# Kernel tuning notes

Measured on AMD Instinct MI355X. Metric: run time of the kernel, lower is better.

The kernel has to match this reference:

```python
import jax, jax.numpy as jnp
import numpy as np

N = 16384      # nodes
E = 524288     # edges (avg degree 32)
F_IN = 128     # input features
H1 = 256       # first_gcn_dimensions
H2 = 256       # second_gcn_dimensions
D1 = 64        # first_dense_neurons
D2 = 2         # second_dense_neurons (fixed by EYE=ones(2))


def setup_inputs() -> dict:
    key = jax.random.key(0)
    ks = jax.random.split(key, 8)
    w = lambda k, shp: (jax.random.normal(k, shp, jnp.float32) * 0.05)
    return dict(
        features=jax.random.normal(ks[0], (N, F_IN), jnp.float32),
        edges=jax.random.randint(ks[1], (2, E), 0, N),
        W1=w(ks[2], (F_IN, H1)), b1=jnp.zeros((H1,), jnp.float32),
        W2=w(ks[3], (H1, H2)), b2=jnp.zeros((H2,), jnp.float32),
        fc1_w=w(ks[4], (D1, H2)), fc1_b=jnp.zeros((D1,), jnp.float32),
        fc2_w=w(ks[5], (D2, D1)), fc2_b=jnp.zeros((D2,), jnp.float32),
    )


def gcn_conv(x, W, b, src, dst, n):
    """PyG GCNConv: xW, add self-loops, symmetric D^-1/2 (A+I) D^-1/2 aggregation."""
    x = x @ W
    loops = jnp.arange(n)
    s = jnp.concatenate([src, loops])
    d = jnp.concatenate([dst, loops])
    deg = jax.ops.segment_sum(jnp.ones(s.shape, x.dtype), d, num_segments=n)
    dinv = jnp.where(deg > 0, jax.lax.rsqrt(deg), 0.0)
    msg = x[s] * (dinv[s] * dinv[d])[:, None]          # gather + scale
    return jax.ops.segment_sum(msg, d, num_segments=n) + b  # scatter-add


def reference(features, edges, W1, b1, W2, b2, fc1_w, fc1_b, fc2_w, fc2_b):
    n = features.shape[0]
    src, dst = edges[0], edges[1]
    h1 = jax.nn.relu(gcn_conv(features, W1, b1, src, dst, n))
    h2 = gcn_conv(h1, W2, b2, src, dst, n)                 # [N, H2]
    a1 = jnp.tanh(h2 @ fc1_w.T + fc1_b)                    # [N, D1]
    assignment = jax.nn.softmax(a1 @ fc2_w.T + fc2_b, axis=1)  # [N, 2]
    group_features = assignment.T @ h2                     # [2, H2]
    # to_dense_adj: dense NxN adjacency, duplicate edges accumulate
    adj = jnp.zeros((n, n), h2.dtype).at[src, dst].add(1.0)
    new_adj = assignment.T @ (adj @ assignment)            # [2, 2]
    positive = jnp.clip(group_features[0][None, :], -100.0, 100.0)
    negative = jnp.clip(group_features[1][None, :], -100.0, 100.0)
    # F.normalize(p=1, dim=1) with eps=1e-12
    denom = jnp.maximum(jnp.sum(jnp.abs(new_adj), axis=1, keepdims=True), 1e-12)
    norm_diag = jnp.diag(new_adj / denom)
    pos_penalty = jnp.mean((norm_diag - 1.0) ** 2)         # MSE vs ones(2)
    graph_embedding = jnp.mean(group_features, axis=0, keepdims=True)  # [1, H2]
    return (graph_embedding, positive, negative, pos_penalty)
```

## Files before the change

### kernel.cpp

```cpp
#include <hip/hip_runtime.h>
#include <hip/hip_bf16.h>
#include <math.h>

#define N_NODES 16384
#define N_EDGES 524288
#define F_IN 128
#define H1 256
#define H2 256
#define D1 64
#define NA_GRID 128
#define DEG_CAP 96

typedef __attribute__((ext_vector_type(8))) short short8;
typedef __attribute__((ext_vector_type(4))) float floatx4;
typedef unsigned short ushort_t;
typedef unsigned int uint_t;

__device__ inline float bf2f(ushort_t u) {
    union { uint_t i; float f; } v;
    v.i = ((uint_t)u) << 16;
    return v.f;
}
__device__ inline float u2f_lo(uint_t u) {
    union { uint_t i; float f; } v;
    v.i = u << 16;
    return v.f;
}
__device__ inline float u2f_hi(uint_t u) {
    union { uint_t i; float f; } v;
    v.i = u & 0xffff0000u;
    return v.f;
}
__device__ inline ushort_t f2bs(float x) {
    __hip_bfloat16 h = __float2bfloat16(x);
    return *reinterpret_cast<ushort_t*>(&h);
}

__global__ __launch_bounds__(256) void prep_fill(
    const int* __restrict__ src, const int* __restrict__ dst,
    const float* __restrict__ W1, const float* __restrict__ W2,
    const float* __restrict__ fc1_w,
    int* __restrict__ cur, int* __restrict__ col,
    ushort_t* __restrict__ W1t, ushort_t* __restrict__ W2t,
    ushort_t* __restrict__ fc1bf) {
    int b = blockIdx.x, t = threadIdx.x;
    if (b < 2048) {
        int e = b * 256 + t;
        int d = dst[e];
        int pos = atomicAdd(&cur[d], 1);
        if (pos < DEG_CAP) col[d * DEG_CAP + pos] = src[e];
    } else if (b < 2176) {
        int idx = (b - 2048) * 256 + t;
        int n = idx >> 7, k = idx & 127;
        W1t[idx] = f2bs(W1[k * 256 + n]);
    } else if (b < 2432) {
        int idx = (b - 2176) * 256 + t;
        int n = idx >> 8, k = idx & 255;
        W2t[idx] = f2bs(W2[k * 256 + n]);
    } else {
        int idx = (b - 2432) * 256 + t;
        fc1bf[idx] = f2bs(fc1_w[idx]);
    }
}

__global__ __launch_bounds__(256) void scale_feat(
    const float* __restrict__ features, const int* __restrict__ cnt,
    ushort_t* __restrict__ zs) {
    int gid = blockIdx.x * 256 + threadIdx.x;
    int node = gid >> 5;
    float d = rsqrtf((float)(cnt[node] + 1));
    float4 v = *(const float4*)&features[gid * 4];
    uint2 p;
    p.x = (uint_t)f2bs(v.x * d) | ((uint_t)f2bs(v.y * d) << 16);
    p.y = (uint_t)f2bs(v.z * d) | ((uint_t)f2bs(v.w * d) << 16);
    *(uint2*)&zs[gid * 4] = p;
}

__global__ __launch_bounds__(512, 8) void fused_layer1(
    const ushort_t* __restrict__ zs, const int* __restrict__ cnt,
    const int* __restrict__ col, const float* __restrict__ b1,
    const ushort_t* __restrict__ W1t, const ushort_t* __restrict__ W2t,
    ushort_t* __restrict__ bufY) {
    __shared__ __align__(16) ushort_t Az[16 * 136];
    __shared__ __align__(16) ushort_t Ah[16 * 264];
    const int tid = threadIdx.x;
    const int lane = tid & 63;
    const int wave = tid >> 6;
    const int m = lane & 15;
    const int quad = lane >> 4;
    const int row0 = blockIdx.x * 16;

    for (int ii = 0; ii < 2; ++ii) {
        const int nl = wave * 2 + ii;
        const int node = __builtin_amdgcn_readfirstlane(row0 + nl);
        const int foff = lane * 2;
        const int deg = __builtin_amdgcn_readfirstlane(cnt[node]);
        uint_t self = *(const uint_t*)&zs[(size_t)node * 128 + foff];
        float a0 = u2f_lo(self);
        float a1 = u2f_hi(self);
        const int s0 = node * DEG_CAP;
        const int s1 = s0 + min(deg, DEG_CAP);
        int base = s0;
        for (; base + 8 <= s1; base += 8) {
            uint_t uu[8];
            #pragma unroll
            for (int q = 0; q < 8; ++q) {
                int j = col[base + q];
                uu[q] = *(const uint_t*)&zs[(size_t)j * 128 + foff];
            }
            #pragma unroll
            for (int q = 0; q < 8; ++q) {
                a0 += u2f_lo(uu[q]);
                a1 += u2f_hi(uu[q]);
            }
        }
        for (; base < s1; ++base) {
            int j = col[base];
            uint_t u = *(const uint_t*)&zs[(size_t)j * 128 + foff];
            a0 += u2f_lo(u);
            a1 += u2f_hi(u);
        }
        float dnode = rsqrtf((float)(deg + 1));
        *(uint_t*)&Az[nl * 136 + foff] =
            (uint_t)f2bs(a0 * dnode) | ((uint_t)f2bs(a1 * dnode) << 16);
    }
    __syncthreads();

    const int wcol0 = wave * 32;
    floatx4 acc[2];
    const floatx4 zero4 = {0.f, 0.f, 0.f, 0.f};
    acc[0] = zero4; acc[1] = zero4;
    #pragma unroll
    for (int k0 = 0; k0 < 128; k0 += 32) {
        short8 a = *(const short8*)&Az[m * 136 + k0 + quad * 8];
        #pragma unroll
        for (int j = 0; j < 2; ++j) {
            short8 bb = *(const short8*)
                &W1t[(size_t)(wcol0 + j * 16 + m) * 128 + k0 + quad * 8];
            acc[j] = __builtin_amdgcn_mfma_f32_16x16x32_bf16(a, bb, acc[j], 0, 0, 0);
        }
    }
    #pragma unroll
    for (int j = 0; j < 2; ++j) {
        int cg = wcol0 + j * 16 + m;
        float bv = b1[cg];
        #pragma unroll
        for (int r = 0; r < 4; ++r) {
            float v = fmaxf(acc[j][r] + bv, 0.0f);
            Ah[(quad * 4 + r) * 264 + cg] = f2bs(v);
        }
    }
    __syncthreads();

    acc[0] = zero4; acc[1] = zero4;
    #pragma unroll
    for (int k0 = 0; k0 < 256; k0 += 32) {
        short8 a = *(const short8*)&Ah[m * 264 + k0 + quad * 8];
        #pragma unroll
        for (int j = 0; j < 2; ++j) {
            short8 bb = *(const short8*)
                &W2t[(size_t)(wcol0 + j * 16 + m) * 256 + k0 + quad * 8];
            acc[j] = __builtin_amdgcn_mfma_f32_16x16x32_bf16(a, bb, acc[j], 0, 0, 0);
        }
    }
    float rs4[4];
    #pragma unroll
    for (int r = 0; r < 4; ++r)
        rs4[r] = rsqrtf((float)(cnt[row0 + quad * 4 + r] + 1));
    #pragma unroll
    for (int j = 0; j < 2; ++j) {
        int cg = wcol0 + j * 16 + m;
        #pragma unroll
        for (int r = 0; r < 4; ++r)
            bufY[(size_t)(row0 + quad * 4 + r) * 256 + cg] = f2bs(acc[j][r] * rs4[r]);
    }
}

__global__ __launch_bounds__(512, 8) void fused_assign(
    const ushort_t* __restrict__ bufY, const int* __restrict__ cnt,
    const int* __restrict__ col, const float* __restrict__ b2,
    const ushort_t* __restrict__ fc1bf, const float* __restrict__ fc1_b,
    const float* __restrict__ fc2_w, const float* __restrict__ fc2_b,
    float* __restrict__ assign, float* __restrict__ gfr) {
    __shared__ __align__(16) ushort_t Ah[16 * 264];
    __shared__ float sha[16][65];
    __shared__ float sas0[16], sas1[16];
    const int tid = threadIdx.x;
    const int lane = tid & 63;
    const int wave = tid >> 6;
    const int m = lane & 15;
    const int quad = lane >> 4;
    const int row0 = blockIdx.x * 16;

    for (int ii = 0; ii < 2; ++ii) {
        const int nl = wave * 2 + ii;
        const int node = __builtin_amdgcn_readfirstlane(row0 + nl);
        const int foff = lane * 4;
        const int deg = __builtin_amdgcn_readfirstlane(cnt[node]);
        float a0, a1, a2, a3;
        {
            uint2 u = *(const uint2*)&bufY[(size_t)node * 256 + foff];
            a0 = u2f_lo(u.x); a1 = u2f_hi(u.x);
            a2 = u2f_lo(u.y); a3 = u2f_hi(u.y);
        }
        const int s0 = node * DEG_CAP;
        const int s1 = s0 + min(deg, DEG_CAP);
        int base = s0;
        for (; base + 8 <= s1; base += 8) {
            uint2 uu[8];
            #pragma unroll
            for (int q = 0; q < 8; ++q) {
                int j = col[base + q];
                uu[q] = *(const uint2*)&bufY[(size_t)j * 256 + foff];
            }
            #pragma unroll
            for (int q = 0; q < 8; ++q) {
                a0 += u2f_lo(uu[q].x); a1 += u2f_hi(uu[q].x);
                a2 += u2f_lo(uu[q].y); a3 += u2f_hi(uu[q].y);
            }
        }
        for (; base < s1; ++base) {
            int j = col[base];
            uint2 u = *(const uint2*)&bufY[(size_t)j * 256 + foff];
            a0 += u2f_lo(u.x); a1 += u2f_hi(u.x);
            a2 += u2f_lo(u.y); a3 += u2f_hi(u.y);
        }
        float di = rsqrtf((float)(deg + 1));
        uint2 pk;
        pk.x = (uint_t)f2bs(a0 * di + b2[foff + 0]) |
               ((uint_t)f2bs(a1 * di + b2[foff + 1]) << 16);
        pk.y = (uint_t)f2bs(a2 * di + b2[foff + 2]) |
               ((uint_t)f2bs(a3 * di + b2[foff + 3]) << 16);
        *(uint2*)&Ah[nl * 264 + foff] = pk;
    }
    __syncthreads();

    if (wave < 4) {
        floatx4 acc = {0.f, 0.f, 0.f, 0.f};
        #pragma unroll
        for (int k0 = 0; k0 < 256; k0 += 32) {
            short8 a = *(const short8*)&Ah[m * 264 + k0 + quad * 8];
            short8 bb = *(const short8*)
                &fc1bf[(size_t)(wave * 16 + m) * 256 + k0 + quad * 8];
            acc = __builtin_amdgcn_mfma_f32_16x16x32_bf16(a, bb, acc, 0, 0, 0);
        }
        int cg = wave * 16 + m;
        float bv = fc1_b[cg];
        #pragma unroll
        for (int r = 0; r < 4; ++r)
            sha[quad * 4 + r][cg] = tanhf(acc[r] + bv);
    }
    __syncthreads();

    if (tid < 16) {
        float p0 = fc2_b[0], p1 = fc2_b[1];
        #pragma unroll 8
        for (int t = 0; t < 64; ++t) {
            float a = sha[tid][t];
            p0 += a * fc2_w[t];
            p1 += a * fc2_w[64 + t];
        }
        float mx = fmaxf(p0, p1);
        float e0 = expf(p0 - mx), e1 = expf(p1 - mx);
        float inv = 1.0f / (e0 + e1);
        float2 as; as.x = e0 * inv; as.y = e1 * inv;
        *(float2*)&assign[(row0 + tid) * 2] = as;
        sas0[tid] = as.x; sas1[tid] = as.y;
    }
    __syncthreads();

    {
        const int f = tid & 255;
        const int which = tid >> 8;
        const float* sv = which ? sas1 : sas0;
        float acc = 0.f;
        #pragma unroll
        for (int i = 0; i < 16; ++i)
            acc += sv[i] * bf2f(Ah[i * 264 + f]);
        float* gfc = gfr + (blockIdx.x & 3) * 512;
        atomicAdd(&gfc[which * 256 + f], acc);
    }
}

__global__ __launch_bounds__(256) void newadj_fin(
    const int* __restrict__ src, const int* __restrict__ dst,
    const float* __restrict__ assign, float* __restrict__ napart,
    int* __restrict__ cntt, const float* __restrict__ gfr,
    float* __restrict__ out) {
    __shared__ float red[4][4];
    __shared__ int sticket;
    const int tid = threadIdx.x;
    const int b = blockIdx.x;
    const int lane = tid & 63;
    const int wave = tid >> 6;

    float a00 = 0.f, a01 = 0.f, a10 = 0.f, a11 = 0.f;
    for (int e = b * 256 + tid; e < N_EDGES; e += NA_GRID * 256) {
        int s = src[e], d = dst[e];
        float s0 = assign[s * 2], s1 = assign[s * 2 + 1];
        float d0 = assign[d * 2], d1 = assign[d * 2 + 1];
        a00 += s0 * d0; a01 += s0 * d1; a10 += s1 * d0; a11 += s1 * d1;
    }
    #pragma unroll
    for (int off = 32; off; off >>= 1) {
        a00 += __shfl_down(a00, off);
        a01 += __shfl_down(a01, off);
        a10 += __shfl_down(a10, off);
        a11 += __shfl_down(a11, off);
    }
    if (lane == 0) {
        red[wave][0] = a00; red[wave][1] = a01;
        red[wave][2] = a10; red[wave][3] = a11;
    }
    __syncthreads();
    if (tid < 4) {
        float v = red[0][tid] + red[1][tid] + red[2][tid] + red[3][tid];
        __hip_atomic_store(&napart[b * 4 + tid], v, __ATOMIC_RELEASE,
                           __HIP_MEMORY_SCOPE_AGENT);
    }
    __syncthreads();
    if (tid == 0)
        sticket = __hip_atomic_fetch_add(cntt, 1, __ATOMIC_ACQ_REL,
                                         __HIP_MEMORY_SCOPE_AGENT);
    __syncthreads();
    if (sticket != NA_GRID - 1) return;

    float acc = 0.f;
    for (int i = lane; i < NA_GRID; i += 64)
        acc += __hip_atomic_load(&napart[i * 4 + wave], __ATOMIC_RELAXED,
                                 __HIP_MEMORY_SCOPE_AGENT);
    #pragma unroll
    for (int off = 32; off; off >>= 1) acc += __shfl_down(acc, off);
    __shared__ float na[4];
    if (lane == 0) na[wave] = acc;
    __syncthreads();
    float g0 = gfr[tid] + gfr[512 + tid] + gfr[1024 + tid] + gfr[1536 + tid];
    float g1 = gfr[256 + tid] + gfr[768 + tid] + gfr[1280 + tid] + gfr[1792 + tid];
    out[tid] = 0.5f * (g0 + g1);
    out[256 + tid] = fminf(fmaxf(g0, -100.f), 100.f);
    out[512 + tid] = fminf(fmaxf(g1, -100.f), 100.f);
    if (tid == 0) {
        float n00 = na[0], n01 = na[1], n10 = na[2], n11 = na[3];
        float den0 = fmaxf(fabsf(n00) + fabsf(n01), 1e-12f);
        float den1 = fmaxf(fabsf(n10) + fabsf(n11), 1e-12f);
        float x0 = n00 / den0 - 1.0f;
        float x1 = n11 / den1 - 1.0f;
        out[768] = 0.5f * (x0 * x0 + x1 * x1);
    }
}


extern "C" void kernel_launch(void* const* d_in, const int* in_sizes, int n_in,
                              void* d_out, int out_size, void* d_ws, size_t ws_size,
                              hipStream_t stream) {
    const float* features = (const float*)d_in[0];
    const int* edges = (const int*)d_in[1];
    const int* src = edges;
    const int* dst = edges + N_EDGES;
    const float* W1 = (const float*)d_in[2];
    const float* b1 = (const float*)d_in[3];
    const float* W2 = (const float*)d_in[4];
    const float* b2 = (const float*)d_in[5];
    const float* fc1_w = (const float*)d_in[6];
    const float* fc1_b = (const float*)d_in[7];
    const float* fc2_w = (const float*)d_in[8];
    const float* fc2_b = (const float*)d_in[9];
    float* out = (float*)d_out;

    char* ws = (char*)d_ws;
    auto carve = [&](size_t bytes) {
        void* q = (void*)ws;
        ws += (bytes + 255) & ~(size_t)255;
        return q;
    };
    int* cur = (int*)carve(N_NODES * 4);
    float* gfr = (float*)carve(4 * 512 * 4);
    int* cnt_na = (int*)carve(256);
    int* col = (int*)carve((size_t)N_NODES * DEG_CAP * 4);
    float* assign = (float*)carve(N_NODES * 2 * 4);
    float* napart = (float*)carve(NA_GRID * 4 * 4);
    ushort_t* fc1bf = (ushort_t*)carve(64 * 256 * 2);
    ushort_t* zs = (ushort_t*)carve((size_t)N_NODES * F_IN * 2);
    ushort_t* W1t = (ushort_t*)carve(256 * 128 * 2);
    ushort_t* W2t = (ushort_t*)carve(256 * 256 * 2);
    ushort_t* bufY = (ushort_t*)carve((size_t)N_NODES * 256 * 2);

    hipMemsetAsync(cur, 0, N_NODES * 4 + 4 * 512 * 4 + 256, stream);

    prep_fill<<<2496, 256, 0, stream>>>(src, dst, W1, W2, fc1_w,
                                        cur, col, W1t, W2t, fc1bf);
    scale_feat<<<2048, 256, 0, stream>>>(features, cur, zs);
    fused_layer1<<<N_NODES / 16, 512, 0, stream>>>(
        zs, cur, col, b1, W1t, W2t, bufY);
    fused_assign<<<N_NODES / 16, 512, 0, stream>>>(
        bufY, cur, col, b2, fc1bf, fc1_b, fc2_w, fc2_b, assign, gfr);
    newadj_fin<<<NA_GRID, 256, 0, stream>>>(src, dst, assign, napart,
                                            cnt_na, gfr, out);
}
```

Baseline: 189.6 us.

## Use 16-bit padded neighbor lists and split layer-2 aggregation into column-half passes

Neighbor indices are stored as 16-bit values and each list is padded to a multiple of 16 with a sentinel node whose feature row is zeroed, so the gather loops run without a remainder and load indices two at a time. The layer-2 aggregation moves out of fused_assign into a separate agg2 kernel that runs twice, once per 128-column half, to shrink each pass's gather working set for cache locality. The result goes through a new h2buf buffer. The newadj grid grows from 128 to 512 blocks. This costs an extra HBM round trip of h2, two more launches, and padded gathers of the zero row.

```diff
diff --git a/kernel.cpp b/kernel.cpp
--- a/kernel.cpp
+++ b/kernel.cpp
@@ -8,8 +8,9 @@
 #define H1 256
 #define H2 256
 #define D1 64
-#define NA_GRID 128
+#define NA_GRID 512
 #define DEG_CAP 96
+#define SENT 16384
 
 typedef __attribute__((ext_vector_type(8))) short short8;
 typedef __attribute__((ext_vector_type(4))) float floatx4;
@@ -35,12 +36,15 @@
     __hip_bfloat16 h = __float2bfloat16(x);
     return *reinterpret_cast<ushort_t*>(&h);
 }
+__device__ inline uint_t pack2(float lo, float hi) {
+    return (uint_t)f2bs(lo) | ((uint_t)f2bs(hi) << 16);
+}
 
 __global__ __launch_bounds__(256) void prep_fill(
     const int* __restrict__ src, const int* __restrict__ dst,
     const float* __restrict__ W1, const float* __restrict__ W2,
     const float* __restrict__ fc1_w,
-    int* __restrict__ cur, int* __restrict__ col,
+    int* __restrict__ cur, ushort_t* __restrict__ col,
     ushort_t* __restrict__ W1t, ushort_t* __restrict__ W2t,
     ushort_t* __restrict__ fc1bf) {
     int b = blockIdx.x, t = threadIdx.x;
@@ -48,7 +52,7 @@
         int e = b * 256 + t;
         int d = dst[e];
         int pos = atomicAdd(&cur[d], 1);
-        if (pos < DEG_CAP) col[d * DEG_CAP + pos] = src[e];
+        if (pos < DEG_CAP) col[d * DEG_CAP + pos] = (ushort_t)src[e];
     } else if (b < 2176) {
         int idx = (b - 2048) * 256 + t;
         int n = idx >> 7, k = idx & 127;
@@ -65,20 +69,36 @@
 
 __global__ __launch_bounds__(256) void scale_feat(
     const float* __restrict__ features, const int* __restrict__ cnt,
-    ushort_t* __restrict__ zs) {
-    int gid = blockIdx.x * 256 + threadIdx.x;
+    ushort_t* __restrict__ zs, ushort_t* __restrict__ bufY,
+    ushort_t* __restrict__ col) {
+    int b = blockIdx.x, t = threadIdx.x;
+    if (b == 2048) {
+        uint4 z4 = {0u, 0u, 0u, 0u};
+        if (t < 16)
+            *(uint4*)&zs[(size_t)SENT * 128 + t * 8] = z4;
+        else if (t >= 64 && t < 96)
+            *(uint4*)&bufY[(size_t)SENT * 256 + (t - 64) * 8] = z4;
+        return;
+    }
+    int gid = b * 256 + t;
     int node = gid >> 5;
-    float d = rsqrtf((float)(cnt[node] + 1));
+    int hl = gid & 31;
+    int deg = cnt[node];
+    float d = rsqrtf((float)(deg + 1));
     float4 v = *(const float4*)&features[gid * 4];
     uint2 p;
-    p.x = (uint_t)f2bs(v.x * d) | ((uint_t)f2bs(v.y * d) << 16);
-    p.y = (uint_t)f2bs(v.z * d) | ((uint_t)f2bs(v.w * d) << 16);
+    p.x = pack2(v.x * d, v.y * d);
+    p.y = pack2(v.z * d, v.w * d);
     *(uint2*)&zs[gid * 4] = p;
+    if (deg < DEG_CAP) {
+        int pad = (16 - (deg & 15)) & 15;
+        if (hl < pad) col[node * DEG_CAP + deg + hl] = (ushort_t)SENT;
+    }
 }
 
 __global__ __launch_bounds__(512, 8) void fused_layer1(
     const ushort_t* __restrict__ zs, const int* __restrict__ cnt,
-    const int* __restrict__ col, const float* __restrict__ b1,
+    const ushort_t* __restrict__ col, const float* __restrict__ b1,
     const ushort_t* __restrict__ W1t, const ushort_t* __restrict__ W2t,
     ushort_t* __restrict__ bufY) {
     __shared__ __align__(16) ushort_t Az[16 * 136];
@@ -89,40 +109,35 @@
     const int m = lane & 15;
     const int quad = lane >> 4;
     const int row0 = blockIdx.x * 16;
+    const uint_t* colu = (const uint_t*)col;
 
     for (int ii = 0; ii < 2; ++ii) {
         const int nl = wave * 2 + ii;
         const int node = __builtin_amdgcn_readfirstlane(row0 + nl);
         const int foff = lane * 2;
-        const int deg = __builtin_amdgcn_readfirstlane(cnt[node]);
+        const int deg = cnt[node];
+        const int nb = (min(deg, DEG_CAP) + 15) >> 4;
         uint_t self = *(const uint_t*)&zs[(size_t)node * 128 + foff];
-        float a0 = u2f_lo(self);
-        float a1 = u2f_hi(self);
-        const int s0 = node * DEG_CAP;
-        const int s1 = s0 + min(deg, DEG_CAP);
-        int base = s0;
-        for (; base + 8 <= s1; base += 8) {
-            uint_t uu[8];
+        float a0 = u2f_lo(self), a1 = u2f_hi(self);
+        const int cb = node * (DEG_CAP / 2);
+        for (int tb = 0; tb < nb; ++tb) {
+            uint_t w[8];
             #pragma unroll
-            for (int q = 0; q < 8; ++q) {
-                int j = col[base + q];
-                uu[q] = *(const uint_t*)&zs[(size_t)j * 128 + foff];
+            for (int k = 0; k < 8; ++k) w[k] = colu[cb + tb * 8 + k];
+            uint_t g[16];
+            #pragma unroll
+            for (int k = 0; k < 8; ++k) {
+                int j0 = w[k] & 0xffff, j1 = w[k] >> 16;
+                g[2 * k]     = *(const uint_t*)&zs[(size_t)j0 * 128 + foff];
+                g[2 * k + 1] = *(const uint_t*)&zs[(size_t)j1 * 128 + foff];
             }
             #pragma unroll
-            for (int q = 0; q < 8; ++q) {
-                a0 += u2f_lo(uu[q]);
-                a1 += u2f_hi(uu[q]);
+            for (int q = 0; q < 16; ++q) {
+                a0 += u2f_lo(g[q]); a1 += u2f_hi(g[q]);
             }
         }
-        for (; base < s1; ++base) {
-            int j = col[base];
-            uint_t u = *(const uint_t*)&zs[(size_t)j * 128 + foff];
-            a0 += u2f_lo(u);
-            a1 += u2f_hi(u);
-        }
-        float dnode = rsqrtf((float)(deg + 1));
-        *(uint_t*)&Az[nl * 136 + foff] =
-            (uint_t)f2bs(a0 * dnode) | ((uint_t)f2bs(a1 * dnode) << 16);
+        float dn = rsqrtf((float)(deg + 1));
+        *(uint_t*)&Az[nl * 136 + foff] = pack2(a0 * dn, a1 * dn);
     }
     __syncthreads();
 
@@ -176,9 +191,44 @@
     }
 }
 
-__global__ __launch_bounds__(512, 8) void fused_assign(
+__global__ __launch_bounds__(512, 8) void agg2(
     const ushort_t* __restrict__ bufY, const int* __restrict__ cnt,
-    const int* __restrict__ col, const float* __restrict__ b2,
+    const ushort_t* __restrict__ col, const float* __restrict__ b2,
+    ushort_t* __restrict__ h2buf, int c0) {
+    const int tid = threadIdx.x;
+    const int lane = tid & 63;
+    const int wave = tid >> 6;
+    const int node = __builtin_amdgcn_readfirstlane(blockIdx.x * 8 + wave);
+    const int coff = c0 + lane * 2;
+    const int deg = cnt[node];
+    const int nb = (min(deg, DEG_CAP) + 15) >> 4;
+    uint_t self = *(const uint_t*)&bufY[(size_t)node * 256 + coff];
+    float a0 = u2f_lo(self), a1 = u2f_hi(self);
+    const uint_t* colu = (const uint_t*)col;
+    const int cb = node * (DEG_CAP / 2);
+    for (int tb = 0; tb < nb; ++tb) {
+        uint_t w[8];
+        #pragma unroll
+        for (int k = 0; k < 8; ++k) w[k] = colu[cb + tb * 8 + k];
+        uint_t g[16];
+        #pragma unroll
+        for (int k = 0; k < 8; ++k) {
+            int j0 = w[k] & 0xffff, j1 = w[k] >> 16;
+            g[2 * k]     = *(const uint_t*)&bufY[(size_t)j0 * 256 + coff];
+            g[2 * k + 1] = *(const uint_t*)&bufY[(size_t)j1 * 256 + coff];
+        }
+        #pragma unroll
+        for (int q = 0; q < 16; ++q) {
+            a0 += u2f_lo(g[q]); a1 += u2f_hi(g[q]);
+        }
+    }
+    float di = rsqrtf((float)(deg + 1));
+    *(uint_t*)&h2buf[(size_t)node * 256 + coff] =
+        pack2(a0 * di + b2[coff], a1 * di + b2[coff + 1]);
+}
+
+__global__ __launch_bounds__(512) void fused_assign(
+    const ushort_t* __restrict__ h2buf,
     const ushort_t* __restrict__ fc1bf, const float* __restrict__ fc1_b,
     const float* __restrict__ fc2_w, const float* __restrict__ fc2_b,
     float* __restrict__ assign, float* __restrict__ gfr) {
@@ -192,46 +242,10 @@
     const int quad = lane >> 4;
     const int row0 = blockIdx.x * 16;
 
-    for (int ii = 0; ii < 2; ++ii) {
-        const int nl = wave * 2 + ii;
-        const int node = __builtin_amdgcn_readfirstlane(row0 + nl);
-        const int foff = lane * 4;
-        const int deg = __builtin_amdgcn_readfirstlane(cnt[node]);
-        float a0, a1, a2, a3;
-        {
-            uint2 u = *(const uint2*)&bufY[(size_t)node * 256 + foff];
-            a0 = u2f_lo(u.x); a1 = u2f_hi(u.x);
-            a2 = u2f_lo(u.y); a3 = u2f_hi(u.y);
-        }
-        const int s0 = node * DEG_CAP;
-        const int s1 = s0 + min(deg, DEG_CAP);
-        int base = s0;
-        for (; base + 8 <= s1; base += 8) {
-            uint2 uu[8];
-            #pragma unroll
-            for (int q = 0; q < 8; ++q) {
-                int j = col[base + q];
-                uu[q] = *(const uint2*)&bufY[(size_t)j * 256 + foff];
-            }
-            #pragma unroll
-            for (int q = 0; q < 8; ++q) {
-                a0 += u2f_lo(uu[q].x); a1 += u2f_hi(uu[q].x);
-                a2 += u2f_lo(uu[q].y); a3 += u2f_hi(uu[q].y);
-            }
-        }
-        for (; base < s1; ++base) {
-            int j = col[base];
-            uint2 u = *(const uint2*)&bufY[(size_t)j * 256 + foff];
-            a0 += u2f_lo(u.x); a1 += u2f_hi(u.x);
-            a2 += u2f_lo(u.y); a3 += u2f_hi(u.y);
-        }
-        float di = rsqrtf((float)(deg + 1));
-        uint2 pk;
-        pk.x = (uint_t)f2bs(a0 * di + b2[foff + 0]) |
-               ((uint_t)f2bs(a1 * di + b2[foff + 1]) << 16);
-        pk.y = (uint_t)f2bs(a2 * di + b2[foff + 2]) |
-               ((uint_t)f2bs(a3 * di + b2[foff + 3]) << 16);
-        *(uint2*)&Ah[nl * 264 + foff] = pk;
+    {
+        int r = tid >> 5, c = (tid & 31) * 8;
+        *(uint4*)&Ah[r * 264 + c] =
+            *(const uint4*)&h2buf[(size_t)(row0 + r) * 256 + c];
     }
     __syncthreads();
 
@@ -376,24 +390,27 @@
     int* cur = (int*)carve(N_NODES * 4);
     float* gfr = (float*)carve(4 * 512 * 4);
     int* cnt_na = (int*)carve(256);
-    int* col = (int*)carve((size_t)N_NODES * DEG_CAP * 4);
+    ushort_t* col = (ushort_t*)carve((size_t)N_NODES * DEG_CAP * 2);
     float* assign = (float*)carve(N_NODES * 2 * 4);
     float* napart = (float*)carve(NA_GRID * 4 * 4);
     ushort_t* fc1bf = (ushort_t*)carve(64 * 256 * 2);
-    ushort_t* zs = (ushort_t*)carve((size_t)N_NODES * F_IN * 2);
+    ushort_t* zs = (ushort_t*)carve((size_t)(N_NODES + 1) * F_IN * 2);
     ushort_t* W1t = (ushort_t*)carve(256 * 128 * 2);
     ushort_t* W2t = (ushort_t*)carve(256 * 256 * 2);
-    ushort_t* bufY = (ushort_t*)carve((size_t)N_NODES * 256 * 2);
+    ushort_t* bufY = (ushort_t*)carve((size_t)(N_NODES + 1) * 256 * 2);
+    ushort_t* h2buf = (ushort_t*)carve((size_t)N_NODES * 256 * 2);
 
     hipMemsetAsync(cur, 0, N_NODES * 4 + 4 * 512 * 4 + 256, stream);
 
     prep_fill<<<2496, 256, 0, stream>>>(src, dst, W1, W2, fc1_w,
                                         cur, col, W1t, W2t, fc1bf);
-    scale_feat<<<2048, 256, 0, stream>>>(features, cur, zs);
+    scale_feat<<<2049, 256, 0, stream>>>(features, cur, zs, bufY, col);
     fused_layer1<<<N_NODES / 16, 512, 0, stream>>>(
         zs, cur, col, b1, W1t, W2t, bufY);
+    agg2<<<N_NODES / 8, 512, 0, stream>>>(bufY, cur, col, b2, h2buf, 0);
+    agg2<<<N_NODES / 8, 512, 0, stream>>>(bufY, cur, col, b2, h2buf, 128);
     fused_assign<<<N_NODES / 16, 512, 0, stream>>>(
-        bufY, cur, col, b2, fc1bf, fc1_b, fc2_w, fc2_b, assign, gfr);
+        h2buf, fc1bf, fc1_b, fc2_w, fc2_b, assign, gfr);
     newadj_fin<<<NA_GRID, 256, 0, stream>>>(src, dst, assign, napart,
                                             cnt_na, gfr, out);
 }
```

Measured after the change: 196.7 us. 1.04x slower.
